# Performance work log

Measured on AMD Instinct MI355X. Metric: run time of the kernel, lower is better.

## Reference

```python
import jax, jax.numpy as jnp
import numpy as np

N, E, G = 20000, 320000, 128
D, H, C, L = 128, 8, 16, 4  # hidden, heads, per-head dim, layers
F_NODE, F_EDGE, T = 9, 3, 10


def _lin_init(key, fan_in, shape):
    return jax.random.normal(key, shape, dtype=jnp.float32) / np.sqrt(fan_in)


def setup_inputs() -> dict:
    key = jax.random.key(0)
    ks = jax.random.split(key, 24)
    inp = {
        "x": jax.random.normal(ks[0], (N, F_NODE), dtype=jnp.float32),
        "edge_index": jax.random.randint(ks[1], (2, E), 0, N),
        "edge_attr": jax.random.normal(ks[2], (E, F_EDGE), dtype=jnp.float32),
        "batch": jnp.sort(jax.random.randint(ks[3], (N,), 0, G)),
        # encoders
        "node_w": _lin_init(ks[4], F_NODE, (F_NODE, D)), "node_b": jnp.zeros((D,), jnp.float32),
        "edge_w": _lin_init(ks[5], F_EDGE, (F_EDGE, D)), "edge_b": jnp.zeros((D,), jnp.float32),
        # per-layer TransformerConv params (stacked over L)
        "Wq": _lin_init(ks[6], D, (L, D, D)), "bq": jnp.zeros((L, D), jnp.float32),
        "Wk": _lin_init(ks[7], D, (L, D, D)), "bk": jnp.zeros((L, D), jnp.float32),
        "Wv": _lin_init(ks[8], D, (L, D, D)), "bv": jnp.zeros((L, D), jnp.float32),
        "We": _lin_init(ks[9], D, (L, D, D)),  # lin_edge (no bias in PyG)
        "Wskip": _lin_init(ks[10], D, (L, D, D)), "bskip": jnp.zeros((L, D), jnp.float32),
        "Wbeta": _lin_init(ks[11], 3 * D, (L, 3 * D)),  # lin_beta (no bias)
        "ln_g": jnp.ones((L, D), jnp.float32), "ln_b": jnp.zeros((L, D), jnp.float32),
        # prediction head
        "h1_w": _lin_init(ks[12], D, (D, D // 2)), "h1_b": jnp.zeros((D // 2,), jnp.float32),
        "h2_w": _lin_init(ks[13], D // 2, (D // 2, T)), "h2_b": jnp.zeros((T,), jnp.float32),
    }
    return inp


def _layer_norm(x, g, b, eps=1e-5):
    mu = jnp.mean(x, -1, keepdims=True)
    var = jnp.mean(jnp.square(x - mu), -1, keepdims=True)
    return (x - mu) * jax.lax.rsqrt(var + eps) * g + b


def _transformer_conv(h, ea, src, dst, Wq, bq, Wk, bk, Wv, bv, We, Wskip, bskip, Wbeta):
    # PyG TransformerConv, concat=True, beta=True, edge_dim=D, eval mode (no dropout)
    q = (h @ Wq + bq)[dst].reshape(E, H, C)           # query at destination i
    k = (h @ Wk + bk)[src].reshape(E, H, C)
    v = (h @ Wv + bv)[src].reshape(E, H, C)
    e = (ea @ We).reshape(E, H, C)
    k = k + e
    alpha = jnp.sum(q * k, -1) / np.sqrt(C)           # [E, H]
    m = jax.ops.segment_max(alpha, dst, num_segments=N)
    alpha = jnp.exp(alpha - m[dst])
    denom = jax.ops.segment_sum(alpha, dst, num_segments=N)
    alpha = alpha / (denom[dst] + 1e-16)
    msg = (v + e) * alpha[..., None]                  # [E, H, C]
    out = jax.ops.segment_sum(msg, dst, num_segments=N).reshape(N, D)
    x_r = h @ Wskip + bskip                           # root/skip transform
    beta = jax.nn.sigmoid(jnp.concatenate([out, x_r, out - x_r], -1) @ Wbeta)  # [N]
    return beta[:, None] * x_r + (1.0 - beta)[:, None] * out


def reference(x, edge_index, edge_attr, batch, node_w, node_b, edge_w, edge_b,
              Wq, bq, Wk, bk, Wv, bv, We, Wskip, bskip, Wbeta, ln_g, ln_b,
              h1_w, h1_b, h2_w, h2_b):
    src, dst = edge_index[0], edge_index[1]
    h = jax.nn.relu(x @ node_w + node_b)              # node encoder + relu
    ea = edge_attr @ edge_w + edge_b                  # edge encoder
    for l in range(L):
        h_res = h
        h = _transformer_conv(h, ea, src, dst, Wq[l], bq[l], Wk[l], bk[l],
                              Wv[l], bv[l], We[l], Wskip[l], bskip[l], Wbeta[l])
        h = _layer_norm(h + h_res, ln_g[l], ln_b[l])
    # global mean pool over graphs
    sums = jax.ops.segment_sum(h, batch, num_segments=G)
    cnt = jax.ops.segment_sum(jnp.ones((N,), h.dtype), batch, num_segments=G)
    pooled = sums / jnp.maximum(cnt, 1.0)[:, None]    # [G, D]
    return jax.nn.relu(pooled @ h1_w + h1_b) @ h2_w + h2_b  # [G, T]
```

## Files before the change

### kernel.cpp

```cpp
#include <hip/hip_runtime.h>
#include <hip/hip_bf16.h>

typedef __hip_bfloat16 bf16;
typedef __attribute__((ext_vector_type(8))) short short8;
typedef __attribute__((ext_vector_type(4))) float f32x4;

#define DEV __device__ __forceinline__

DEV float blo(unsigned u) { return __uint_as_float(u << 16); }
DEV float bhi(unsigned u) { return __uint_as_float(u & 0xffff0000u); }

DEV float waveReduceSum(float v) {
#pragma unroll
    for (int m = 1; m < 64; m <<= 1) v += __shfl_xor(v, m);
    return v;
}

__global__ __launch_bounds__(256) void pack_w_k(
    const float* __restrict__ Wq, const float* __restrict__ Wk,
    const float* __restrict__ Wv, const float* __restrict__ Ws,
    bf16* __restrict__ outp, int L) {
    int t = blockIdx.x * 256 + threadIdx.x;
    if (t >= 4 * L * 16384) return;
    int p = t & 16383;
    int ls = t >> 14;
    int l = ls >> 2, s = ls & 3;
    int j = p & 7, ln = (p >> 3) & 63, kb = (p >> 9) & 3, nb = p >> 11;
    int k = kb * 32 + (ln >> 4) * 8 + j;
    int n = nb * 16 + (ln & 15);
    const float* W = (s == 0) ? Wq : (s == 1) ? Wk : (s == 2) ? Wv : Ws;
    outp[t] = __float2bfloat16(W[(size_t)l * 16384 + k * 128 + n]);
}

__global__ __launch_bounds__(256) void pack_b_k(
    const float* __restrict__ bq, const float* __restrict__ bk,
    const float* __restrict__ bv, const float* __restrict__ bs,
    float* __restrict__ outp, int L) {
    int t = blockIdx.x * 256 + threadIdx.x;
    if (t >= 4 * L * 128) return;
    int d = t & 127;
    int ls = t >> 7;
    int l = ls >> 2, s = ls & 3;
    const float* B = (s == 0) ? bq : (s == 1) ? bk : (s == 2) ? bv : bs;
    outp[t] = B[l * 128 + d];
}

__global__ __launch_bounds__(256) void edge_mats_k(
    const float* __restrict__ edge_w, const float* __restrict__ edge_b,
    const float* __restrict__ We, float* __restrict__ Me, int L) {
    int t = blockIdx.x * 256 + threadIdx.x;
    if (t >= L * 4 * 128) return;
    int n = t & 127, j = (t >> 7) & 3, l = t >> 9;
    const float* W = We + (size_t)l * 16384;
    const float* row = (j < 3) ? (edge_w + j * 128) : edge_b;
    float acc = 0.f;
    for (int d = 0; d < 128; ++d) acc += row[d] * W[d * 128 + n];
    Me[t] = acc;
}

__global__ __launch_bounds__(256) void hist_k(const int* __restrict__ ei,
                                              int* __restrict__ deg, int E) {
    int e = blockIdx.x * 256 + threadIdx.x;
    if (e >= E) return;
    atomicAdd(&deg[ei[E + e]], 1);
}

__global__ __launch_bounds__(1024) void scan_k(const int* __restrict__ deg,
                                               int* __restrict__ off,
                                               int* __restrict__ cursor, int N, int E) {
    __shared__ int part[1024];
    int t = threadIdx.x;
    int chunk = (N + 1023) >> 10;
    int lo = t * chunk, hi = min(lo + chunk, N);
    int s = 0;
    for (int i = lo; i < hi; ++i) s += deg[i];
    part[t] = s;
    __syncthreads();
    for (int d = 1; d < 1024; d <<= 1) {
        int v = (t >= d) ? part[t - d] : 0;
        __syncthreads();
        part[t] += v;
        __syncthreads();
    }
    int base = (t == 0) ? 0 : part[t - 1];
    for (int i = lo; i < hi; ++i) {
        off[i] = base;
        cursor[i] = base;
        base += deg[i];
    }
    if (t == 1023) off[N] = E;
}

__global__ __launch_bounds__(256) void fill_k(const int* __restrict__ ei,
                                              const float* __restrict__ eattr,
                                              int* __restrict__ cursor,
                                              int* __restrict__ el_src,
                                              float4* __restrict__ ea4, int E) {
    int e = blockIdx.x * 256 + threadIdx.x;
    if (e >= E) return;
    int dst = ei[E + e];
    int pos = atomicAdd(&cursor[dst], 1);
    el_src[pos] = ei[e];
    ea4[pos] = make_float4(eattr[e * 3], eattr[e * 3 + 1], eattr[e * 3 + 2], 0.f);
}

__global__ __launch_bounds__(256) void node_enc_k(
    const float* __restrict__ x, const float* __restrict__ w,
    const float* __restrict__ b, float* __restrict__ h,
    bf16* __restrict__ h_bf, int N) {
    int t = blockIdx.x * 256 + threadIdx.x;
    if (t >= N * 128) return;
    int n = t >> 7, d = t & 127;
    float acc = b[d];
#pragma unroll
    for (int i = 0; i < 9; ++i) acc += x[n * 9 + i] * w[i * 128 + d];
    float r = fmaxf(acc, 0.f);
    h[t] = r;
    h_bf[t] = __float2bfloat16(r);
}

__global__ __launch_bounds__(256) void qkvs_k(
    const bf16* __restrict__ A, const bf16* __restrict__ Wp,
    const float* __restrict__ bp,
    bf16* __restrict__ Q, bf16* __restrict__ kvb,
    float* __restrict__ S, int M) {
    int tid = threadIdx.x;
    int l = tid & 63, w = tid >> 6;
    int row0 = blockIdx.x * 64;
    const short* Ab = (const short*)A + (size_t)(row0 + (l & 15)) * 128 + ((l >> 4) * 8);
    short8 a[4][4];
#pragma unroll
    for (int mb = 0; mb < 4; ++mb)
#pragma unroll
        for (int kb = 0; kb < 4; ++kb)
            a[mb][kb] = *(const short8*)(Ab + mb * 16 * 128 + kb * 32);
    int colb = w * 32 + (l & 15);
#pragma unroll
    for (int s = 0; s < 4; ++s) {
        const short* Wb = (const short*)Wp + s * 16384;
        short8 bfr[2][4];
#pragma unroll
        for (int nbi = 0; nbi < 2; ++nbi)
#pragma unroll
            for (int kb = 0; kb < 4; ++kb)
                bfr[nbi][kb] = *(const short8*)(Wb + (size_t)(((w * 2 + nbi) * 4 + kb) * 64 + l) * 8);
        f32x4 acc[4][2] = {};
#pragma unroll
        for (int kb = 0; kb < 4; ++kb)
#pragma unroll
            for (int mb = 0; mb < 4; ++mb)
#pragma unroll
                for (int nbi = 0; nbi < 2; ++nbi)
                    acc[mb][nbi] = __builtin_amdgcn_mfma_f32_16x16x32_bf16(
                        a[mb][kb], bfr[nbi][kb], acc[mb][nbi], 0, 0, 0);
        float bias0 = bp[s * 128 + colb];
        float bias1 = bp[s * 128 + colb + 16];
#pragma unroll
        for (int mb = 0; mb < 4; ++mb) {
            int rbase = row0 + mb * 16 + (l >> 4) * 4;
#pragma unroll
            for (int j = 0; j < 4; ++j) {
                int r = rbase + j;
                if (r >= M) continue;
#pragma unroll
                for (int nbi = 0; nbi < 2; ++nbi) {
                    int c = colb + nbi * 16;
                    float v = acc[mb][nbi][j] + (nbi ? bias1 : bias0);
                    if (s == 0) {
                        Q[(size_t)r * 128 + c] = __float2bfloat16(v);
                    } else if (s == 3) {
                        S[(size_t)r * 128 + c] = v;
                    } else {
                        size_t idx = ((size_t)r * 64 + (c >> 1)) * 4 + (c & 1) + ((s == 2) ? 2 : 0);
                        kvb[idx] = __float2bfloat16(v);
                    }
                }
            }
        }
    }
}

__global__ __launch_bounds__(256) void attn_k(
    const int* __restrict__ off, const int* __restrict__ el_src,
    const float4* __restrict__ ea4, const float* __restrict__ Me,
    const bf16* __restrict__ Q, const bf16* __restrict__ kvb,
    const float* __restrict__ S,
    float* __restrict__ h, bf16* __restrict__ h_bf,
    const float* __restrict__ Wb, const float* __restrict__ lng,
    const float* __restrict__ lnb, int N) {
    int gw = (blockIdx.x * 256 + threadIdx.x) >> 6;
    int l = threadIdx.x & 63;
    int nw = (gridDim.x * 256) >> 6;
    int d0 = 2 * l, d1 = 2 * l + 1;
    float m00 = Me[d0],       m01 = Me[d1];
    float m10 = Me[128 + d0], m11 = Me[128 + d1];
    float m20 = Me[256 + d0], m21 = Me[256 + d1];
    float mb0 = Me[384 + d0], mb1 = Me[384 + d1];
    float wba0 = Wb[d0],       wba1 = Wb[d1];
    float wbb0 = Wb[128 + d0], wbb1 = Wb[128 + d1];
    float wbc0 = Wb[256 + d0], wbc1 = Wb[256 + d1];
    float g0 = lng[d0], g1 = lng[d1];
    float bb0 = lnb[d0], bb1 = lnb[d1];
    const unsigned* Q2 = (const unsigned*)Q;
    const uint2* KV2 = (const uint2*)kvb;
    for (int n = gw; n < N; n += nw) {
        unsigned q2 = Q2[(size_t)n * 64 + l];
        float q0 = blo(q2) * 0.25f, q1 = bhi(q2) * 0.25f;
        float acc0 = 0.f, acc1 = 0.f, den = 0.f;
        int i0 = off[n], i1 = off[n + 1];
        int src_n = (i0 < i1) ? el_src[i0] : 0;
        float4 ae_n = (i0 < i1) ? ea4[i0] : make_float4(0, 0, 0, 0);
        for (int i = i0; i < i1; ++i) {
            int src = src_n;
            float4 aeb = ae_n;
            if (i + 1 < i1) {
                src_n = el_src[i + 1];
                ae_n = ea4[i + 1];
            }
            uint2 kv = KV2[(size_t)src * 64 + l];
            float e0 = fmaf(aeb.x, m00, fmaf(aeb.y, m10, fmaf(aeb.z, m20, mb0)));
            float e1 = fmaf(aeb.x, m01, fmaf(aeb.y, m11, fmaf(aeb.z, m21, mb1)));
            float s = q0 * (blo(kv.x) + e0) + q1 * (bhi(kv.x) + e1);
            s += __shfl_xor(s, 1);
            s += __shfl_xor(s, 2);
            s += __shfl_xor(s, 4);
            float p = __expf(s);
            den += p;
            acc0 += (blo(kv.y) + e0) * p;
            acc1 += (bhi(kv.y) + e1) * p;
        }
        float inv = den > 0.f ? 1.f / den : 0.f;
        float o0 = acc0 * inv, o1 = acc1 * inv;
        size_t base = (size_t)n * 128;
        float s0 = S[base + d0], s1 = S[base + d1];
        float part = o0 * wba0 + s0 * wbb0 + (o0 - s0) * wbc0
                   + o1 * wba1 + s1 * wbb1 + (o1 - s1) * wbc1;
        float g = waveReduceSum(part);
        float beta = 1.f / (1.f + __expf(-g));
        float y0 = beta * s0 + (1.f - beta) * o0;
        float y1 = beta * s1 + (1.f - beta) * o1;
        float z0 = y0 + h[base + d0];
        float z1 = y1 + h[base + d1];
        float mean = waveReduceSum(z0 + z1) * (1.f / 128.f);
        float c0 = z0 - mean, c1 = z1 - mean;
        float var = waveReduceSum(c0 * c0 + c1 * c1) * (1.f / 128.f);
        float invs = rsqrtf(var + 1e-5f);
        float r0 = c0 * invs * g0 + bb0;
        float r1 = c1 * invs * g1 + bb1;
        h[base + d0] = r0;
        h[base + d1] = r1;
        h_bf[base + d0] = __float2bfloat16(r0);
        h_bf[base + d1] = __float2bfloat16(r1);
    }
}

__global__ __launch_bounds__(128) void pool_head_k(
    const float* __restrict__ h, const int* __restrict__ batch,
    const float* __restrict__ h1w, const float* __restrict__ h1b,
    const float* __restrict__ h2w, const float* __restrict__ h2b,
    float* __restrict__ out, int N) {
    int g = blockIdx.x;
    int t = threadIdx.x;
    auto lb = [&](int val) {
        int lo = 0, hi = N;
        while (lo < hi) {
            int mid = (lo + hi) >> 1;
            if (batch[mid] < val) lo = mid + 1; else hi = mid;
        }
        return lo;
    };
    int s = lb(g), e = lb(g + 1);
    __shared__ float pl[128];
    __shared__ float hid[64];
    float acc = 0.f;
    for (int n = s; n < e; ++n) acc += h[(size_t)n * 128 + t];
    float cnt = fmaxf((float)(e - s), 1.f);
    pl[t] = acc / cnt;
    __syncthreads();
    if (t < 64) {
        float a = h1b[t];
        for (int k = 0; k < 128; ++k) a += pl[k] * h1w[k * 64 + t];
        hid[t] = fmaxf(a, 0.f);
    }
    __syncthreads();
    if (t < 10) {
        float o = h2b[t];
        for (int k = 0; k < 64; ++k) o += hid[k] * h2w[k * 10 + t];
        out[g * 10 + t] = o;
    }
}

extern "C" void kernel_launch(void* const* d_in, const int* in_sizes, int n_in,
                              void* d_out, int out_size, void* d_ws, size_t ws_size,
                              hipStream_t stream) {
    const float* x      = (const float*)d_in[0];
    const int*   ei     = (const int*)d_in[1];
    const float* eattr  = (const float*)d_in[2];
    const int*   batch  = (const int*)d_in[3];
    const float* node_w = (const float*)d_in[4];
    const float* node_b = (const float*)d_in[5];
    const float* edge_w = (const float*)d_in[6];
    const float* edge_b = (const float*)d_in[7];
    const float* Wq     = (const float*)d_in[8];
    const float* bq     = (const float*)d_in[9];
    const float* Wk     = (const float*)d_in[10];
    const float* bk     = (const float*)d_in[11];
    const float* Wv     = (const float*)d_in[12];
    const float* bv     = (const float*)d_in[13];
    const float* We     = (const float*)d_in[14];
    const float* Wskip  = (const float*)d_in[15];
    const float* bskip  = (const float*)d_in[16];
    const float* Wbeta  = (const float*)d_in[17];
    const float* ln_g   = (const float*)d_in[18];
    const float* ln_b   = (const float*)d_in[19];
    const float* h1_w   = (const float*)d_in[20];
    const float* h1_b   = (const float*)d_in[21];
    const float* h2_w   = (const float*)d_in[22];
    const float* h2_b   = (const float*)d_in[23];
    float* out = (float*)d_out;

    const int N = in_sizes[3];
    const int E = in_sizes[2] / 3;
    const int L = in_sizes[8] / 16384;
    const int G = out_size / 10;

    char* wptr = (char*)d_ws;
    auto alloc = [&](size_t bytes) {
        char* p = wptr;
        wptr += (bytes + 255) & ~(size_t)255;
        return p;
    };
    float* h      = (float*)alloc((size_t)(N + 64) * 128 * 4);
    bf16*  h_bf   = (bf16*)alloc((size_t)(N + 64) * 128 * 2);
    bf16*  Qb     = (bf16*)alloc((size_t)(N + 64) * 128 * 2);
    bf16*  kvb    = (bf16*)alloc((size_t)(N + 64) * 256 * 2);
    float* S      = (float*)alloc((size_t)(N + 64) * 128 * 4);
    float4* ea4   = (float4*)alloc((size_t)E * 16);
    bf16*  Wpack  = (bf16*)alloc((size_t)4 * L * 16384 * 2);
    float* bpack  = (float*)alloc((size_t)4 * L * 128 * 4);
    float* Me     = (float*)alloc((size_t)L * 4 * 128 * 4);
    int*   deg    = (int*)alloc((size_t)N * 4);
    int*   off    = (int*)alloc((size_t)(N + 1) * 4);
    int*   cursor = (int*)alloc((size_t)N * 4);
    int*   el_src = (int*)alloc((size_t)E * 4);

    dim3 b256(256), b128(128);

    pack_w_k<<<(4 * L * 16384 + 255) / 256, b256, 0, stream>>>(Wq, Wk, Wv, Wskip, Wpack, L);
    pack_b_k<<<(4 * L * 128 + 255) / 256, b256, 0, stream>>>(bq, bk, bv, bskip, bpack, L);
    edge_mats_k<<<(L * 4 * 128 + 255) / 256, b256, 0, stream>>>(edge_w, edge_b, We, Me, L);
    hipMemsetAsync(deg, 0, (size_t)N * 4, stream);
    hist_k<<<(E + 255) / 256, b256, 0, stream>>>(ei, deg, E);
    scan_k<<<1, 1024, 0, stream>>>(deg, off, cursor, N, E);
    fill_k<<<(E + 255) / 256, b256, 0, stream>>>(ei, eattr, cursor, el_src, ea4, E);
    node_enc_k<<<(N * 128 + 255) / 256, b256, 0, stream>>>(x, node_w, node_b, h, h_bf, N);

    int gN = (N + 63) / 64;
    int gAttn = (N + 3) / 4;
    for (int l = 0; l < L; ++l) {
        qkvs_k<<<gN, b256, 0, stream>>>(h_bf, Wpack + (size_t)l * 4 * 16384,
                                        bpack + (size_t)l * 4 * 128, Qb, kvb, S, N);
        attn_k<<<gAttn, b256, 0, stream>>>(off, el_src, ea4, Me + (size_t)l * 512,
                                           Qb, kvb, S, h, h_bf,
                                           Wbeta + (size_t)l * 384,
                                           ln_g + (size_t)l * 128, ln_b + (size_t)l * 128, N);
    }

    pool_head_k<<<G, b128, 0, stream>>>(h, batch, h1_w, h1_b, h2_w, h2_b, out, N);
}
```

Before: 400.1 us.

## Prefetch next-edge KV gather in attention and parallelize mean pooling with atomics

The attention loop now issues the K/V gather for the next edge alongside its index and edge-attribute loads, so the dependent gather latency overlaps with the current edge's math. The single-pass pooling, where one block walks each graph's nodes serially, is split into a partial-sum kernel over 64-node chunks that uses atomics into per-graph sums, plus a small head kernel. This spreads pooling across many more blocks in exchange for an extra memset, an extra launch, and float atomics whose summation order is nondeterministic.

```diff
diff --git a/kernel.cpp b/kernel.cpp
--- a/kernel.cpp
+++ b/kernel.cpp
@@ -208,18 +208,23 @@
         float q0 = blo(q2) * 0.25f, q1 = bhi(q2) * 0.25f;
         float acc0 = 0.f, acc1 = 0.f, den = 0.f;
         int i0 = off[n], i1 = off[n + 1];
-        int src_n = (i0 < i1) ? el_src[i0] : 0;
-        float4 ae_n = (i0 < i1) ? ea4[i0] : make_float4(0, 0, 0, 0);
+        uint2 kv = make_uint2(0, 0);
+        float4 ae = make_float4(0, 0, 0, 0);
+        if (i0 < i1) {
+            int src0 = el_src[i0];
+            ae = ea4[i0];
+            kv = KV2[(size_t)src0 * 64 + l];
+        }
         for (int i = i0; i < i1; ++i) {
-            int src = src_n;
-            float4 aeb = ae_n;
+            uint2 kvN = make_uint2(0, 0);
+            float4 aeN = make_float4(0, 0, 0, 0);
             if (i + 1 < i1) {
-                src_n = el_src[i + 1];
-                ae_n = ea4[i + 1];
+                int srcN = el_src[i + 1];
+                aeN = ea4[i + 1];
+                kvN = KV2[(size_t)srcN * 64 + l];
             }
-            uint2 kv = KV2[(size_t)src * 64 + l];
-            float e0 = fmaf(aeb.x, m00, fmaf(aeb.y, m10, fmaf(aeb.z, m20, mb0)));
-            float e1 = fmaf(aeb.x, m01, fmaf(aeb.y, m11, fmaf(aeb.z, m21, mb1)));
+            float e0 = fmaf(ae.x, m00, fmaf(ae.y, m10, fmaf(ae.z, m20, mb0)));
+            float e1 = fmaf(ae.x, m01, fmaf(ae.y, m11, fmaf(ae.z, m21, mb1)));
             float s = q0 * (blo(kv.x) + e0) + q1 * (bhi(kv.x) + e1);
             s += __shfl_xor(s, 1);
             s += __shfl_xor(s, 2);
@@ -228,6 +233,8 @@
             den += p;
             acc0 += (blo(kv.y) + e0) * p;
             acc1 += (bhi(kv.y) + e1) * p;
+            kv = kvN;
+            ae = aeN;
         }
         float inv = den > 0.f ? 1.f / den : 0.f;
         float o0 = acc0 * inv, o1 = acc1 * inv;
@@ -254,8 +261,29 @@
     }
 }
 
-__global__ __launch_bounds__(128) void pool_head_k(
+__global__ __launch_bounds__(256) void pool_partial_k(
     const float* __restrict__ h, const int* __restrict__ batch,
+    float* __restrict__ psum, int N) {
+    int d = threadIdx.x & 127;
+    int half = threadIdx.x >> 7;
+    int n0 = blockIdx.x * 64;
+    int n1 = min(n0 + 64, N);
+    float acc = 0.f;
+    int curg = -1;
+    for (int n = n0 + half; n < n1; n += 2) {
+        int g = batch[n];
+        if (g != curg) {
+            if (curg >= 0) atomicAdd(&psum[curg * 128 + d], acc);
+            acc = 0.f;
+            curg = g;
+        }
+        acc += h[(size_t)n * 128 + d];
+    }
+    if (curg >= 0) atomicAdd(&psum[curg * 128 + d], acc);
+}
+
+__global__ __launch_bounds__(128) void head2_k(
+    const float* __restrict__ psum, const int* __restrict__ batch,
     const float* __restrict__ h1w, const float* __restrict__ h1b,
     const float* __restrict__ h2w, const float* __restrict__ h2b,
     float* __restrict__ out, int N) {
@@ -270,12 +298,10 @@
         return lo;
     };
     int s = lb(g), e = lb(g + 1);
+    float cnt = fmaxf((float)(e - s), 1.f);
     __shared__ float pl[128];
     __shared__ float hid[64];
-    float acc = 0.f;
-    for (int n = s; n < e; ++n) acc += h[(size_t)n * 128 + t];
-    float cnt = fmaxf((float)(e - s), 1.f);
-    pl[t] = acc / cnt;
+    pl[t] = psum[g * 128 + t] / cnt;
     __syncthreads();
     if (t < 64) {
         float a = h1b[t];
@@ -343,6 +369,7 @@
     int*   off    = (int*)alloc((size_t)(N + 1) * 4);
     int*   cursor = (int*)alloc((size_t)N * 4);
     int*   el_src = (int*)alloc((size_t)E * 4);
+    float* psum   = (float*)alloc((size_t)G * 128 * 4);
 
     dim3 b256(256), b128(128);
 
@@ -366,5 +393,7 @@
                                            ln_g + (size_t)l * 128, ln_b + (size_t)l * 128, N);
     }
 
-    pool_head_k<<<G, b128, 0, stream>>>(h, batch, h1_w, h1_b, h2_w, h2_b, out, N);
-}
+    hipMemsetAsync(psum, 0, (size_t)G * 128 * 4, stream);
+    pool_partial_k<<<gN, b256, 0, stream>>>(h, batch, psum, N);
+    head2_k<<<G, b128, 0, stream>>>(psum, batch, h1_w, h1_b, h2_w, h2_b, out, N);
+}
```

Result: slower. 418.0 us (+4.5%).
